# Optimization experiments

Hardware: AMD Instinct MI355X
Metric: run time of the kernel (lower is better)

Reference implementation:

```python
import jax, jax.numpy as jnp
import numpy as np

B, L, H, E, D = 4, 2048, 8, 64, 64  # seq S == L (causal mask requires square scores)


def setup_inputs() -> dict:
    key = jax.random.key(0)
    k0, k1, k2, k3, k4 = jax.random.split(key, 5)
    queries = jax.random.normal(k0, (B, L, H, E), jnp.float32)
    keys = jax.random.normal(k1, (B, L, H, E), jnp.float32)
    values = jax.random.normal(k2, (B, L, H, D), jnp.float32)
    # per-sample learned de-stationary scale (positive) and bias
    tau = jax.random.uniform(k3, (B, 1, 1), jnp.float32, 0.5, 1.5)
    delta = jax.random.normal(k4, (B, 1, L), jnp.float32) * 0.1
    return {"queries": queries, "keys": keys, "values": values, "tau": tau, "delta": delta}


def reference(queries, keys, values, tau, delta):
    Bq, Lq, Hq, Eq = queries.shape
    S = keys.shape[1]
    scale = 1.0 / jnp.sqrt(jnp.asarray(Eq, jnp.float32))
    # torch path: rearrange('b s h d l -> (b d) s h l') with s=h=d=1 -> [B,1,1,1] / [B,1,1,S]
    tau_b = tau.reshape(Bq, 1, 1, 1)
    delta_b = delta.reshape(Bq, 1, 1, -1)[..., :S]
    # scores: [B, H, L, S]
    scores = jnp.einsum('blhe,bshe->bhls', queries, keys) * tau_b + delta_b
    causal = jnp.triu(jnp.ones((Lq, S), bool), k=1)  # True above diagonal -> masked
    scores = jnp.where(causal, -jnp.inf, scores)
    A = jax.nn.softmax(scale * scores, axis=-1)  # dropout is identity in eval/reference
    V = jnp.einsum('bhls,bshd->blhd', A, values)  # [B, L, H, D]
    return V
```

## Files before the change

kernel.cpp:

```cpp
#include <hip/hip_runtime.h>
#include <hip/hip_bf16.h>

#define Bsz 4
#define Lsz 2048
#define Hsz 8

typedef __attribute__((ext_vector_type(8))) short bf16x8;
typedef __attribute__((ext_vector_type(4))) short bf16x4;
typedef __attribute__((ext_vector_type(4))) float f32x4;

__device__ __forceinline__ short f2bs(float f) {
    union { float f; unsigned u; } v; v.f = f;
    unsigned r = v.u + 0x7FFFu + ((v.u >> 16) & 1u);
    return (short)(r >> 16);
}
__device__ __forceinline__ short f2bs_rh(float f) {
    return (short)((__float_as_uint(f) + 0x8000u) >> 16);
}

__device__ __forceinline__ void stage16(const short* g, short* l) {
    __builtin_amdgcn_global_load_lds(
        (const __attribute__((address_space(1))) unsigned int*)g,
        (__attribute__((address_space(3))) unsigned int*)l,
        16, 0, 0);
}

__global__ __launch_bounds__(256) void prep_kv(
    const float* __restrict__ ksrc, const float* __restrict__ vsrc,
    short* __restrict__ Kf, short* __restrict__ Vf)
{
    __shared__ float Tl[64][65];
    const int raw = blockIdx.x;
    const int tid = threadIdx.x;
    const bool isK = raw < Bsz*Hsz*32;
    const int bid = isK ? raw : raw - Bsz*Hsz*32;
    const int tl = bid & 31, bh = bid >> 5;
    const int b = bh >> 3, h = bh & 7;

    const int row = tid >> 2, c0 = (tid & 3) * 16;
    const float* src = (isK ? ksrc : vsrc)
                     + (((size_t)b*Lsz + tl*64 + row)*Hsz + h)*64 + c0;
    *(float4*)&Tl[row][c0]      = *(const float4*)(src);
    *(float4*)&Tl[row][c0 + 4]  = *(const float4*)(src + 4);
    *(float4*)&Tl[row][c0 + 8]  = *(const float4*)(src + 8);
    *(float4*)&Tl[row][c0 + 12] = *(const float4*)(src + 12);
    __syncthreads();

    const int lane = tid & 63, ln = lane & 15, quad = lane >> 4;
    if (isK) {
        short* dst = Kf + (size_t)bid * 4096;
        #pragma unroll
        for (int cc = 0; cc < 2; ++cc) {
            const int c  = (tid >> 6)*2 + cc;
            const int nt = c >> 1, eh = c & 1;
            const float* rp = &Tl[nt*16 + ln][eh*32 + quad*8];
            bf16x8 o = {f2bs(rp[0]),f2bs(rp[1]),f2bs(rp[2]),f2bs(rp[3]),
                        f2bs(rp[4]),f2bs(rp[5]),f2bs(rp[6]),f2bs(rp[7])};
            *(bf16x8*)(dst + c*512 + lane*8) = o;
        }
    } else {
        short* dst = Vf + (size_t)bid * 4096;
        #pragma unroll
        for (int cc = 0; cc < 2; ++cc) {
            const int cp  = (tid >> 6)*2 + cc;
            const int m16 = cp >> 1, nt0 = (cp & 1)*2;
            const int d   = m16*16 + ln;
            const int s0  = nt0*16 + quad*4;
            bf16x8 o = {f2bs(Tl[s0+0][d]),  f2bs(Tl[s0+1][d]),
                        f2bs(Tl[s0+2][d]),  f2bs(Tl[s0+3][d]),
                        f2bs(Tl[s0+16][d]), f2bs(Tl[s0+17][d]),
                        f2bs(Tl[s0+18][d]), f2bs(Tl[s0+19][d])};
            *(bf16x8*)(dst + cp*512 + lane*8) = o;
        }
    }
}

__global__ __launch_bounds__(256, 2) void dsattn_main(
    const float* __restrict__ q,
    const short* __restrict__ Kf,
    const short* __restrict__ Vf,
    const float* __restrict__ tau,
    const float* __restrict__ delta,
    float* __restrict__ out)
{
    __shared__ __align__(16) short Kb[2][4096];
    __shared__ __align__(16) short Vb[2][4096];
    __shared__ float dls[Lsz];

    const int tid  = threadIdx.x;
    const int wv   = tid >> 6;
    const int lane = tid & 63;
    const int ln   = lane & 15;
    const int quad = lane >> 4;

    const int bh = blockIdx.x;
    const int b  = bh >> 3, h = bh & 7;
    const int j  = blockIdx.y;
    const int qt = (j < 8) ? j : 23 - j;
    const int q0 = qt * 128;
    const int T  = 2*qt + 2;
    const int Tw = (wv < 2) ? T - 1 : T;

    const float c2  = 0.125f * 1.44269504f;
    const float st2 = c2 * tau[b];

    const short* kt = Kf + (size_t)bh * (32*4096);
    const short* vt = Vf + (size_t)bh * (32*4096);

    {
        const float* dsrc = delta + (size_t)b*Lsz + tid*8;
        float4 a = *(const float4*)(dsrc);
        float4 c = *(const float4*)(dsrc + 4);
        a.x*=c2; a.y*=c2; a.z*=c2; a.w*=c2;
        c.x*=c2; c.y*=c2; c.z*=c2; c.w*=c2;
        *(float4*)&dls[tid*8]     = a;
        *(float4*)&dls[tid*8 + 4] = c;
    }

    #pragma unroll
    for (int u = 0; u < 4; ++u) {
        const int c = wv*4 + u;
        const short* g = ((c < 8) ? kt : vt) + (c & 7)*512 + lane*8;
        short* l = ((c < 8) ? &Kb[0][0] : &Vb[0][0]) + (c & 7)*512;
        stage16(g, l);
    }

    bf16x8 qf[2][2];
    #pragma unroll
    for (int hh = 0; hh < 2; ++hh) {
        const float* qrow = q + (((size_t)b*Lsz + q0 + wv*32 + hh*16 + ln)*Hsz + h)*64;
        float4 a0 = *(const float4*)(qrow + quad*8);
        float4 a1 = *(const float4*)(qrow + quad*8 + 4);
        float4 b0 = *(const float4*)(qrow + 32 + quad*8);
        float4 b1 = *(const float4*)(qrow + 32 + quad*8 + 4);
        qf[hh][0] = (bf16x8){f2bs(a0.x),f2bs(a0.y),f2bs(a0.z),f2bs(a0.w),
                             f2bs(a1.x),f2bs(a1.y),f2bs(a1.z),f2bs(a1.w)};
        qf[hh][1] = (bf16x8){f2bs(b0.x),f2bs(b0.y),f2bs(b0.z),f2bs(b0.w),
                             f2bs(b1.x),f2bs(b1.y),f2bs(b1.z),f2bs(b1.w)};
    }

    f32x4 oacc[2][4];
    #pragma unroll
    for (int hh = 0; hh < 2; ++hh)
        #pragma unroll
        for (int m = 0; m < 4; ++m) oacc[hh][m] = (f32x4){0.f,0.f,0.f,0.f};
    float l_acc[2] = {0.f, 0.f};

    __syncthreads();

    for (int t = 0; t < T; ++t) {
        const int cur = t & 1;
        if (t + 1 < T) {
            const int nb = cur ^ 1;
            #pragma unroll
            for (int u = 0; u < 4; ++u) {
                const int c = wv*4 + u;
                const short* g = ((c < 8) ? kt : vt)
                               + (size_t)(t+1)*4096 + (c & 7)*512 + lane*8;
                short* l = ((c < 8) ? &Kb[nb][0] : &Vb[nb][0]) + (c & 7)*512;
                stage16(g, l);
            }
        }

        if (t < Tw) {
            const short* Kc = &Kb[cur][0];
            const short* Vc = &Vb[cur][0];
            const int k0 = t*64;

            f32x4 sacc[2][4];
            #pragma unroll
            for (int nt = 0; nt < 4; ++nt) {
                bf16x8 kf0 = *(const bf16x8*)(Kc + (nt*2+0)*512 + lane*8);
                bf16x8 kf1 = *(const bf16x8*)(Kc + (nt*2+1)*512 + lane*8);
                #pragma unroll
                for (int hh = 0; hh < 2; ++hh) {
                    f32x4 z = (f32x4){0.f,0.f,0.f,0.f};
                    z = __builtin_amdgcn_mfma_f32_16x16x32_bf16(kf0, qf[hh][0], z, 0,0,0);
                    sacc[hh][nt] = __builtin_amdgcn_mfma_f32_16x16x32_bf16(kf1, qf[hh][1], z, 0,0,0);
                }
            }

            f32x4 dlv[4];
            #pragma unroll
            for (int nt = 0; nt < 4; ++nt)
                dlv[nt] = *(const f32x4*)&dls[k0 + nt*16 + quad*4];

            bf16x4 pT[2][4];
            #pragma unroll
            for (int hh = 0; hh < 2; ++hh) {
                const int qmin = q0 + wv*32 + hh*16;
                if (k0 + 63 > qmin) {
                    const int qrow = qmin + ln;
                    #pragma unroll
                    for (int nt = 0; nt < 4; ++nt)
                        #pragma unroll
                        for (int r = 0; r < 4; ++r)
                            if (k0 + nt*16 + quad*4 + r > qrow) sacc[hh][nt][r] = -1e30f;
                }
                #pragma unroll
                for (int nt = 0; nt < 4; ++nt) {
                    float p0 = __builtin_amdgcn_exp2f(fmaf(sacc[hh][nt][0], st2, dlv[nt][0]));
                    float p1 = __builtin_amdgcn_exp2f(fmaf(sacc[hh][nt][1], st2, dlv[nt][1]));
                    float p2 = __builtin_amdgcn_exp2f(fmaf(sacc[hh][nt][2], st2, dlv[nt][2]));
                    float p3 = __builtin_amdgcn_exp2f(fmaf(sacc[hh][nt][3], st2, dlv[nt][3]));
                    l_acc[hh] += (p0 + p1) + (p2 + p3);
                    pT[hh][nt] = (bf16x4){f2bs_rh(p0), f2bs_rh(p1), f2bs_rh(p2), f2bs_rh(p3)};
                }
            }

            #pragma unroll
            for (int ntp = 0; ntp < 2; ++ntp)
                #pragma unroll
                for (int m16 = 0; m16 < 4; ++m16) {
                    bf16x8 vv = *(const bf16x8*)(Vc + (m16*2+ntp)*512 + lane*8);
                    bf16x4 v0 = (bf16x4){vv[0], vv[1], vv[2], vv[3]};
                    bf16x4 v1 = (bf16x4){vv[4], vv[5], vv[6], vv[7]};
                    #pragma unroll
                    for (int hh = 0; hh < 2; ++hh) {
                        oacc[hh][m16] = __builtin_amdgcn_mfma_f32_16x16x16bf16_1k(
                            v0, pT[hh][2*ntp+0], oacc[hh][m16], 0,0,0);
                        oacc[hh][m16] = __builtin_amdgcn_mfma_f32_16x16x16bf16_1k(
                            v1, pT[hh][2*ntp+1], oacc[hh][m16], 0,0,0);
                    }
                }
        }

        __syncthreads();
    }

    #pragma unroll
    for (int hh = 0; hh < 2; ++hh) {
        float lsum = l_acc[hh];
        lsum += __shfl_xor(lsum, 16, 64);
        lsum += __shfl_xor(lsum, 32, 64);
        const float inv = 1.0f / lsum;
        const int qrow = q0 + wv*32 + hh*16 + ln;
        float* orow = out + (((size_t)b*Lsz + qrow)*Hsz + h)*64;
        #pragma unroll
        for (int m16 = 0; m16 < 4; ++m16) {
            float4 o = {oacc[hh][m16][0]*inv, oacc[hh][m16][1]*inv,
                        oacc[hh][m16][2]*inv, oacc[hh][m16][3]*inv};
            *(float4*)(orow + m16*16 + quad*4) = o;
        }
    }
}

extern "C" void kernel_launch(void* const* d_in, const int* in_sizes, int n_in,
                              void* d_out, int out_size, void* d_ws, size_t ws_size,
                              hipStream_t stream) {
    (void)in_sizes; (void)n_in; (void)out_size; (void)ws_size;
    const float* q     = (const float*)d_in[0];
    const float* k     = (const float*)d_in[1];
    const float* v     = (const float*)d_in[2];
    const float* tau   = (const float*)d_in[3];
    const float* delta = (const float*)d_in[4];
    float* out = (float*)d_out;

    short* Kf = (short*)d_ws;
    short* Vf = (short*)d_ws + (size_t)(4*1024*1024);

    prep_kv<<<dim3(Bsz*Hsz*32*2), dim3(256), 0, stream>>>(k, v, Kf, Vf);
    dsattn_main<<<dim3(Bsz*Hsz, 16), dim3(256), 0, stream>>>(q, Kf, Vf, tau, delta, out);
}
```

Before: 134.8 us.

## Shrink query tile to 64 rows per block and double grid, raise occupancy

Each block now handles 64 query rows (16 per wave) instead of 128, so the grid has twice as many blocks. The causal tile ordering is rebalanced across four groups, and launch bounds are raised to 4 blocks per SM. Each wave carries half the accumulators, which lowers register pressure and helps hide latency. In exchange, every K/V tile is loaded into shared memory twice as often per query row, and there are more synchronisations per unit of work.

Result: faster. 128.6 us (-4.6%).

```diff
diff --git a/kernel.cpp b/kernel.cpp
--- a/kernel.cpp
+++ b/kernel.cpp
@@ -75,7 +75,7 @@
     }
 }
 
-__global__ __launch_bounds__(256, 2) void dsattn_main(
+__global__ __launch_bounds__(256, 4) void dsattn_main(
     const float* __restrict__ q,
     const short* __restrict__ Kf,
     const short* __restrict__ Vf,
@@ -95,11 +95,11 @@
 
     const int bh = blockIdx.x;
     const int b  = bh >> 3, h = bh & 7;
-    const int j  = blockIdx.y;
-    const int qt = (j < 8) ? j : 23 - j;
-    const int q0 = qt * 128;
-    const int T  = 2*qt + 2;
-    const int Tw = (wv < 2) ? T - 1 : T;
+    const int j  = blockIdx.y, aj = j & 7, gj = j >> 3;
+    const int qt = (gj == 0) ? aj : (gj == 1) ? 15 - aj
+                 : (gj == 2) ? 16 + aj : 31 - aj;
+    const int q0 = qt * 64;
+    const int T  = qt + 1;
 
     const float c2  = 0.125f * 1.44269504f;
     const float st2 = c2 * tau[b];
@@ -125,26 +125,23 @@
         stage16(g, l);
     }
 
-    bf16x8 qf[2][2];
-    #pragma unroll
-    for (int hh = 0; hh < 2; ++hh) {
-        const float* qrow = q + (((size_t)b*Lsz + q0 + wv*32 + hh*16 + ln)*Hsz + h)*64;
+    bf16x8 qf0, qf1;
+    {
+        const float* qrow = q + (((size_t)b*Lsz + q0 + wv*16 + ln)*Hsz + h)*64;
         float4 a0 = *(const float4*)(qrow + quad*8);
         float4 a1 = *(const float4*)(qrow + quad*8 + 4);
         float4 b0 = *(const float4*)(qrow + 32 + quad*8);
         float4 b1 = *(const float4*)(qrow + 32 + quad*8 + 4);
-        qf[hh][0] = (bf16x8){f2bs(a0.x),f2bs(a0.y),f2bs(a0.z),f2bs(a0.w),
-                             f2bs(a1.x),f2bs(a1.y),f2bs(a1.z),f2bs(a1.w)};
-        qf[hh][1] = (bf16x8){f2bs(b0.x),f2bs(b0.y),f2bs(b0.z),f2bs(b0.w),
-                             f2bs(b1.x),f2bs(b1.y),f2bs(b1.z),f2bs(b1.w)};
-    }
-
-    f32x4 oacc[2][4];
+        qf0 = (bf16x8){f2bs(a0.x),f2bs(a0.y),f2bs(a0.z),f2bs(a0.w),
+                       f2bs(a1.x),f2bs(a1.y),f2bs(a1.z),f2bs(a1.w)};
+        qf1 = (bf16x8){f2bs(b0.x),f2bs(b0.y),f2bs(b0.z),f2bs(b0.w),
+                       f2bs(b1.x),f2bs(b1.y),f2bs(b1.z),f2bs(b1.w)};
+    }
+
+    f32x4 oacc[4];
     #pragma unroll
-    for (int hh = 0; hh < 2; ++hh)
-        #pragma unroll
-        for (int m = 0; m < 4; ++m) oacc[hh][m] = (f32x4){0.f,0.f,0.f,0.f};
-    float l_acc[2] = {0.f, 0.f};
+    for (int m = 0; m < 4; ++m) oacc[m] = (f32x4){0.f,0.f,0.f,0.f};
+    float l_acc = 0.f;
 
     __syncthreads();
 
@@ -162,86 +159,71 @@
             }
         }
 
-        if (t < Tw) {
-            const short* Kc = &Kb[cur][0];
-            const short* Vc = &Vb[cur][0];
-            const int k0 = t*64;
-
-            f32x4 sacc[2][4];
-            #pragma unroll
-            for (int nt = 0; nt < 4; ++nt) {
-                bf16x8 kf0 = *(const bf16x8*)(Kc + (nt*2+0)*512 + lane*8);
-                bf16x8 kf1 = *(const bf16x8*)(Kc + (nt*2+1)*512 + lane*8);
-                #pragma unroll
-                for (int hh = 0; hh < 2; ++hh) {
-                    f32x4 z = (f32x4){0.f,0.f,0.f,0.f};
-                    z = __builtin_amdgcn_mfma_f32_16x16x32_bf16(kf0, qf[hh][0], z, 0,0,0);
-                    sacc[hh][nt] = __builtin_amdgcn_mfma_f32_16x16x32_bf16(kf1, qf[hh][1], z, 0,0,0);
-                }
-            }
-
-            f32x4 dlv[4];
+        const short* Kc = &Kb[cur][0];
+        const short* Vc = &Vb[cur][0];
+        const int k0 = t*64;
+
+        f32x4 sacc[4];
+        #pragma unroll
+        for (int nt = 0; nt < 4; ++nt) {
+            bf16x8 kf0 = *(const bf16x8*)(Kc + (nt*2+0)*512 + lane*8);
+            bf16x8 kf1 = *(const bf16x8*)(Kc + (nt*2+1)*512 + lane*8);
+            f32x4 z = (f32x4){0.f,0.f,0.f,0.f};
+            z = __builtin_amdgcn_mfma_f32_16x16x32_bf16(kf0, qf0, z, 0,0,0);
+            sacc[nt] = __builtin_amdgcn_mfma_f32_16x16x32_bf16(kf1, qf1, z, 0,0,0);
+        }
+
+        f32x4 dlv[4];
+        #pragma unroll
+        for (int nt = 0; nt < 4; ++nt)
+            dlv[nt] = *(const f32x4*)&dls[k0 + nt*16 + quad*4];
+
+        if (t == qt) {
+            const int qrow = q0 + wv*16 + ln;
             #pragma unroll
             for (int nt = 0; nt < 4; ++nt)
-                dlv[nt] = *(const f32x4*)&dls[k0 + nt*16 + quad*4];
-
-            bf16x4 pT[2][4];
+                #pragma unroll
+                for (int r = 0; r < 4; ++r)
+                    if (k0 + nt*16 + quad*4 + r > qrow) sacc[nt][r] = -1e30f;
+        }
+        bf16x4 pT[4];
+        #pragma unroll
+        for (int nt = 0; nt < 4; ++nt) {
+            float p0 = __builtin_amdgcn_exp2f(fmaf(sacc[nt][0], st2, dlv[nt][0]));
+            float p1 = __builtin_amdgcn_exp2f(fmaf(sacc[nt][1], st2, dlv[nt][1]));
+            float p2 = __builtin_amdgcn_exp2f(fmaf(sacc[nt][2], st2, dlv[nt][2]));
+            float p3 = __builtin_amdgcn_exp2f(fmaf(sacc[nt][3], st2, dlv[nt][3]));
+            l_acc += (p0 + p1) + (p2 + p3);
+            pT[nt] = (bf16x4){f2bs_rh(p0), f2bs_rh(p1), f2bs_rh(p2), f2bs_rh(p3)};
+        }
+
+        #pragma unroll
+        for (int ntp = 0; ntp < 2; ++ntp)
             #pragma unroll
-            for (int hh = 0; hh < 2; ++hh) {
-                const int qmin = q0 + wv*32 + hh*16;
-                if (k0 + 63 > qmin) {
-                    const int qrow = qmin + ln;
-                    #pragma unroll
-                    for (int nt = 0; nt < 4; ++nt)
-                        #pragma unroll
-                        for (int r = 0; r < 4; ++r)
-                            if (k0 + nt*16 + quad*4 + r > qrow) sacc[hh][nt][r] = -1e30f;
-                }
-                #pragma unroll
-                for (int nt = 0; nt < 4; ++nt) {
-                    float p0 = __builtin_amdgcn_exp2f(fmaf(sacc[hh][nt][0], st2, dlv[nt][0]));
-                    float p1 = __builtin_amdgcn_exp2f(fmaf(sacc[hh][nt][1], st2, dlv[nt][1]));
-                    float p2 = __builtin_amdgcn_exp2f(fmaf(sacc[hh][nt][2], st2, dlv[nt][2]));
-                    float p3 = __builtin_amdgcn_exp2f(fmaf(sacc[hh][nt][3], st2, dlv[nt][3]));
-                    l_acc[hh] += (p0 + p1) + (p2 + p3);
-                    pT[hh][nt] = (bf16x4){f2bs_rh(p0), f2bs_rh(p1), f2bs_rh(p2), f2bs_rh(p3)};
-                }
+            for (int m16 = 0; m16 < 4; ++m16) {
+                bf16x8 vv = *(const bf16x8*)(Vc + (m16*2+ntp)*512 + lane*8);
+                bf16x4 v0 = (bf16x4){vv[0], vv[1], vv[2], vv[3]};
+                bf16x4 v1 = (bf16x4){vv[4], vv[5], vv[6], vv[7]};
+                oacc[m16] = __builtin_amdgcn_mfma_f32_16x16x16bf16_1k(
+                    v0, pT[2*ntp+0], oacc[m16], 0,0,0);
+                oacc[m16] = __builtin_amdgcn_mfma_f32_16x16x16bf16_1k(
+                    v1, pT[2*ntp+1], oacc[m16], 0,0,0);
             }
 
-            #pragma unroll
-            for (int ntp = 0; ntp < 2; ++ntp)
-                #pragma unroll
-                for (int m16 = 0; m16 < 4; ++m16) {
-                    bf16x8 vv = *(const bf16x8*)(Vc + (m16*2+ntp)*512 + lane*8);
-                    bf16x4 v0 = (bf16x4){vv[0], vv[1], vv[2], vv[3]};
-                    bf16x4 v1 = (bf16x4){vv[4], vv[5], vv[6], vv[7]};
-                    #pragma unroll
-                    for (int hh = 0; hh < 2; ++hh) {
-                        oacc[hh][m16] = __builtin_amdgcn_mfma_f32_16x16x16bf16_1k(
-                            v0, pT[hh][2*ntp+0], oacc[hh][m16], 0,0,0);
-                        oacc[hh][m16] = __builtin_amdgcn_mfma_f32_16x16x16bf16_1k(
-                            v1, pT[hh][2*ntp+1], oacc[hh][m16], 0,0,0);
-                    }
-                }
-        }
-
         __syncthreads();
     }
 
+    float lsum = l_acc;
+    lsum += __shfl_xor(lsum, 16, 64);
+    lsum += __shfl_xor(lsum, 32, 64);
+    const float inv = 1.0f / lsum;
+    const int qrow = q0 + wv*16 + ln;
+    float* orow = out + (((size_t)b*Lsz + qrow)*Hsz + h)*64;
     #pragma unroll
-    for (int hh = 0; hh < 2; ++hh) {
-        float lsum = l_acc[hh];
-        lsum += __shfl_xor(lsum, 16, 64);
-        lsum += __shfl_xor(lsum, 32, 64);
-        const float inv = 1.0f / lsum;
-        const int qrow = q0 + wv*32 + hh*16 + ln;
-        float* orow = out + (((size_t)b*Lsz + qrow)*Hsz + h)*64;
-        #pragma unroll
-        for (int m16 = 0; m16 < 4; ++m16) {
-            float4 o = {oacc[hh][m16][0]*inv, oacc[hh][m16][1]*inv,
-                        oacc[hh][m16][2]*inv, oacc[hh][m16][3]*inv};
-            *(float4*)(orow + m16*16 + quad*4) = o;
-        }
+    for (int m16 = 0; m16 < 4; ++m16) {
+        float4 o = {oacc[m16][0]*inv, oacc[m16][1]*inv,
+                    oacc[m16][2]*inv, oacc[m16][3]*inv};
+        *(float4*)(orow + m16*16 + quad*4) = o;
     }
 }
 
@@ -260,5 +242,5 @@
     short* Vf = (short*)d_ws + (size_t)(4*1024*1024);
 
     prep_kv<<<dim3(Bsz*Hsz*32*2), dim3(256), 0, stream>>>(k, v, Kf, Vf);
-    dsattn_main<<<dim3(Bsz*Hsz, 16), dim3(256), 0, stream>>>(q, Kf, Vf, tau, delta, out);
-}
+    dsattn_main<<<dim3(Bsz*Hsz, 32), dim3(256), 0, stream>>>(q, Kf, Vf, tau, delta, out);
+}
```
